# Optimization experiments

Hardware: AMD Instinct MI355X
Metric: run time of the kernel (lower is better)

Reference implementation:

```python
import jax, jax.numpy as jnp
import numpy as np

NUM_DST = 99
TUNNELS_PER_DST = 8
TOTAL_TUNNELS = NUM_DST * TUNNELS_PER_DST  # 792
NUM_LINKS = 16
BATCH = 65536
# static destination index of each tunnel (from group_sizes = [8]*99)
DEST_OF_TUNNEL = np.repeat(np.arange(NUM_DST), TUNNELS_PER_DST)  # [792]


def setup_inputs() -> dict:
    key = jax.random.key(0)
    k1, k2, k3, k4 = jax.random.split(key, 4)
    pred_ratios = jax.random.uniform(k1, (BATCH, TOTAL_TUNNELS), dtype=jnp.float32)
    demands = jax.random.uniform(k2, (BATCH, NUM_DST), dtype=jnp.float32)
    tunnel_to_link = jax.random.randint(k3, (TOTAL_TUNNELS,), 0, NUM_LINKS)
    link_capacities = jax.random.uniform(k4, (NUM_LINKS,), dtype=jnp.float32)
    return {
        "pred_ratios": pred_ratios,
        "demands": demands,
        "tunnel_to_link": tunnel_to_link,
        "link_capacities": link_capacities,
    }


def reference(pred_ratios, demands, tunnel_to_link, link_capacities):
    # per-tunnel traffic = demand of its destination * predicted split ratio
    tunnel_traffic = pred_ratios * demands[:, DEST_OF_TUNNEL]  # [B, T]
    # vectorized scatter-add over tunnels into links (replaces nested Python loops)
    link_traffic = jnp.zeros((pred_ratios.shape[0], NUM_LINKS), dtype=pred_ratios.dtype)
    link_traffic = link_traffic.at[:, tunnel_to_link].add(tunnel_traffic)  # [B, L]
    link_utilization = link_traffic / (link_capacities[None, :] + 1e-8)
    variance_loss = jnp.var(link_utilization, axis=1, ddof=1).mean()  # torch.var is unbiased
    max_util_loss = jnp.max(link_utilization, axis=1).mean()
    return variance_loss + 0.5 * max_util_loss
```

## Files before the change

kernel.cpp:

```cpp
#include <hip/hip_runtime.h>

#define T      792
#define ND     99
#define NL     16
#define KBLK   25
#define BATCH  65536
#define NTILES (BATCH / 16)

typedef __attribute__((ext_vector_type(8))) short  short8;
typedef __attribute__((ext_vector_type(4))) float  float4v;

__device__ inline unsigned short f2bf(float x) {
    union { float f; unsigned u; } c; c.f = x;
    unsigned r = (c.u + 0x7FFFu + ((c.u >> 16) & 1u)) >> 16;
    return (unsigned short)r;
}

__global__ __launch_bounds__(256) void llb_mfma(
    const float* __restrict__ pred,
    const float* __restrict__ dem,
    const int*   __restrict__ t2l,
    const float* __restrict__ cap,
    float* __restrict__ partial)
{
    __shared__ short8 Bfrag[KBLK][64];

    const int lane = threadIdx.x & 63;
    const int wid  = threadIdx.x >> 6;
    const int g    = lane >> 4;
    const int n    = lane & 15;

    for (int kb = wid; kb < KBLK; kb += 4) {
        const int k0 = kb * 32 + g * 8;
        union { unsigned short us[8]; short8 v; } b;
#pragma unroll
        for (int j = 0; j < 8; ++j) {
            const int k = k0 + j;
            const int link = (k < T) ? t2l[k] : -1;
            b.us[j] = (link == n) ? (unsigned short)0x3F80 : (unsigned short)0;
        }
        Bfrag[kb][lane] = b.v;
    }
    __syncthreads();

    const float invcap = 1.0f / (cap[n] + 1e-8f);

    const int tile = (int)blockIdx.x * 4 + wid;
    const int arow_i = tile * 16 + n;
    const float* __restrict__ arow = pred + (size_t)arow_i * T;
    const float* __restrict__ drow = dem  + (size_t)arow_i * ND;

    float4v acc = {0.f, 0.f, 0.f, 0.f};
#pragma unroll 5
    for (int kb = 0; kb < KBLK; ++kb) {
        const int k0 = kb * 32 + g * 8;
        const int kc = (k0 <= T - 8) ? k0 : (T - 8);
        int d0 = k0 >> 3;
        if (d0 > ND - 1) d0 = ND - 1;

        const float4v a0 = *(const float4v*)(arow + kc);
        const float4v a1 = *(const float4v*)(arow + kc + 4);
        const float   d  = drow[d0];

        union { unsigned short us[8]; short8 v; } af;
        af.us[0] = f2bf(a0.x * d); af.us[1] = f2bf(a0.y * d);
        af.us[2] = f2bf(a0.z * d); af.us[3] = f2bf(a0.w * d);
        af.us[4] = f2bf(a1.x * d); af.us[5] = f2bf(a1.y * d);
        af.us[6] = f2bf(a1.z * d); af.us[7] = f2bf(a1.w * d);

        acc = __builtin_amdgcn_mfma_f32_16x16x32_bf16(af.v, Bfrag[kb][lane], acc, 0, 0, 0);
    }

    float lsum = 0.f;
#pragma unroll
    for (int r = 0; r < 4; ++r) {
        const float u = acc[r] * invcap;
        float s = u, q = u * u, m = u;
#pragma unroll
        for (int off = 8; off >= 1; off >>= 1) {
            s += __shfl_xor(s, off, 16);
            q += __shfl_xor(q, off, 16);
            const float om = __shfl_xor(m, off, 16);
            m = m > om ? m : om;
        }
        if (n == 0) {
            const float var = (q - s * s * (1.0f / 16.0f)) * (1.0f / 15.0f);
            lsum += var + 0.5f * m;
        }
    }
    lsum += __shfl_xor(lsum, 16, 64);
    lsum += __shfl_xor(lsum, 32, 64);
    if (lane == 0) partial[tile] = lsum;
}

__global__ __launch_bounds__(256) void llb_reduce(
    const float* __restrict__ partial, float* __restrict__ out)
{
    float s = 0.f;
    for (int i = threadIdx.x; i < NTILES; i += 256) s += partial[i];
#pragma unroll
    for (int off = 32; off >= 1; off >>= 1) s += __shfl_xor(s, off, 64);
    __shared__ float red[4];
    if ((threadIdx.x & 63) == 0) red[threadIdx.x >> 6] = s;
    __syncthreads();
    if (threadIdx.x == 0)
        out[0] = (red[0] + red[1] + red[2] + red[3]) * (1.0f / (float)BATCH);
}

extern "C" void kernel_launch(void* const* d_in, const int* in_sizes, int n_in,
                              void* d_out, int out_size, void* d_ws, size_t ws_size,
                              hipStream_t stream) {
    const float* pred = (const float*)d_in[0];
    const float* dem  = (const float*)d_in[1];
    const int*   t2l  = (const int*)d_in[2];
    const float* cap  = (const float*)d_in[3];
    float* out     = (float*)d_out;
    float* partial = (float*)d_ws;

    llb_mfma<<<NTILES / 4, 256, 0, stream>>>(pred, dem, t2l, cap, partial);
    llb_reduce<<<1, 256, 0, stream>>>(partial, out);
}
```

Baseline: 324.1 us.

## Split K across wave pairs and pack tunnel-link map into nibbles

Each 16-row tile is now handled by two wavefronts, each covering half of the K blocks. The partial accumulators are combined through shared memory before the variance/max epilogue, and the grid size doubles. The one-hot B fragment is no longer held in shared memory; it is rebuilt in registers from a 4-bit-packed link map. This aims to expose more memory-level parallelism on a bandwidth-bound stream, at the cost of an extra block barrier, per-iteration compare ALU work, and half the waves idling in the epilogue.

Measured after the change: 319.4 us. No clear change (-1.4%).

```diff
diff --git a/kernel.cpp b/kernel.cpp
--- a/kernel.cpp
+++ b/kernel.cpp
@@ -12,8 +12,7 @@
 
 __device__ inline unsigned short f2bf(float x) {
     union { float f; unsigned u; } c; c.f = x;
-    unsigned r = (c.u + 0x7FFFu + ((c.u >> 16) & 1u)) >> 16;
-    return (unsigned short)r;
+    return (unsigned short)((c.u + 0x7FFFu + ((c.u >> 16) & 1u)) >> 16);
 }
 
 __global__ __launch_bounds__(256) void llb_mfma(
@@ -23,74 +22,84 @@
     const float* __restrict__ cap,
     float* __restrict__ partial)
 {
-    __shared__ short8 Bfrag[KBLK][64];
+    __shared__ unsigned packed[KBLK * 4];
+    __shared__ float4v  comb[2][64];
 
     const int lane = threadIdx.x & 63;
     const int wid  = threadIdx.x >> 6;
     const int g    = lane >> 4;
     const int n    = lane & 15;
 
-    for (int kb = wid; kb < KBLK; kb += 4) {
-        const int k0 = kb * 32 + g * 8;
-        union { unsigned short us[8]; short8 v; } b;
+    if (threadIdx.x < KBLK * 4) {
+        const int w = threadIdx.x;
+        unsigned u = 0;
 #pragma unroll
         for (int j = 0; j < 8; ++j) {
-            const int k = k0 + j;
-            const int link = (k < T) ? t2l[k] : -1;
-            b.us[j] = (link == n) ? (unsigned short)0x3F80 : (unsigned short)0;
+            const int k = w * 8 + j;
+            const unsigned link = (k < T) ? (unsigned)t2l[k] : 0u;
+            u |= link << (4 * j);
         }
-        Bfrag[kb][lane] = b.v;
+        packed[w] = u;
     }
     __syncthreads();
 
-    const float invcap = 1.0f / (cap[n] + 1e-8f);
-
-    const int tile = (int)blockIdx.x * 4 + wid;
+    const int tile   = (int)blockIdx.x * 2 + (wid >> 1);
+    const int kb0    = (wid & 1) ? 13 : 0;
+    const int kb1    = (wid & 1) ? KBLK : 13;
     const int arow_i = tile * 16 + n;
     const float* __restrict__ arow = pred + (size_t)arow_i * T;
     const float* __restrict__ drow = dem  + (size_t)arow_i * ND;
 
     float4v acc = {0.f, 0.f, 0.f, 0.f};
-#pragma unroll 5
-    for (int kb = 0; kb < KBLK; ++kb) {
-        const int k0 = kb * 32 + g * 8;
-        const int kc = (k0 <= T - 8) ? k0 : (T - 8);
-        int d0 = k0 >> 3;
-        if (d0 > ND - 1) d0 = ND - 1;
-
+#pragma unroll 4
+    for (int kb = kb0; kb < kb1; ++kb) {
+        const int idx = kb * 4 + g;
+        const int k0  = idx * 8;
+        const int kc  = (k0 <= T - 8) ? k0 : (T - 8);
         const float4v a0 = *(const float4v*)(arow + kc);
         const float4v a1 = *(const float4v*)(arow + kc + 4);
-        const float   d  = drow[d0];
+        const float   d  = (idx < ND) ? drow[idx] : 0.f;
+        const unsigned u = packed[idx];
 
-        union { unsigned short us[8]; short8 v; } af;
+        union { unsigned short us[8]; short8 v; } af, bf;
         af.us[0] = f2bf(a0.x * d); af.us[1] = f2bf(a0.y * d);
         af.us[2] = f2bf(a0.z * d); af.us[3] = f2bf(a0.w * d);
         af.us[4] = f2bf(a1.x * d); af.us[5] = f2bf(a1.y * d);
         af.us[6] = f2bf(a1.z * d); af.us[7] = f2bf(a1.w * d);
+#pragma unroll
+        for (int j = 0; j < 8; ++j)
+            bf.us[j] = (((u >> (4 * j)) & 15u) == (unsigned)n)
+                           ? (unsigned short)0x3F80 : (unsigned short)0;
 
-        acc = __builtin_amdgcn_mfma_f32_16x16x32_bf16(af.v, Bfrag[kb][lane], acc, 0, 0, 0);
+        acc = __builtin_amdgcn_mfma_f32_16x16x32_bf16(af.v, bf.v, acc, 0, 0, 0);
     }
 
-    float lsum = 0.f;
+    if (wid & 1) comb[wid >> 1][lane] = acc;
+    __syncthreads();
+    if (!(wid & 1)) {
+        const float4v o = comb[wid >> 1][lane];
+        const float invcap = 1.0f / (cap[n] + 1e-8f);
+        float lsum = 0.f;
 #pragma unroll
-    for (int r = 0; r < 4; ++r) {
-        const float u = acc[r] * invcap;
-        float s = u, q = u * u, m = u;
+        for (int r = 0; r < 4; ++r) {
+            const float uu = (acc[r] + o[r]) * invcap;
+            float s = uu, q = uu * uu, m = uu;
 #pragma unroll
-        for (int off = 8; off >= 1; off >>= 1) {
-            s += __shfl_xor(s, off, 16);
-            q += __shfl_xor(q, off, 16);
-            const float om = __shfl_xor(m, off, 16);
-            m = m > om ? m : om;
+            for (int off = 8; off >= 1; off >>= 1) {
+                s += __shfl_xor(s, off, 16);
+                q += __shfl_xor(q, off, 16);
+                const float om = __shfl_xor(m, off, 16);
+                m = m > om ? m : om;
+            }
+            if (n == 0) {
+                const float var = (q - s * s * (1.0f / 16.0f)) * (1.0f / 15.0f);
+                lsum += var + 0.5f * m;
+            }
         }
-        if (n == 0) {
-            const float var = (q - s * s * (1.0f / 16.0f)) * (1.0f / 15.0f);
-            lsum += var + 0.5f * m;
-        }
+        lsum += __shfl_xor(lsum, 16, 64);
+        lsum += __shfl_xor(lsum, 32, 64);
+        if (lane == 0) partial[tile] = lsum;
     }
-    lsum += __shfl_xor(lsum, 16, 64);
-    lsum += __shfl_xor(lsum, 32, 64);
-    if (lane == 0) partial[tile] = lsum;
 }
 
 __global__ __launch_bounds__(256) void llb_reduce(
@@ -117,6 +126,6 @@
     float* out     = (float*)d_out;
     float* partial = (float*)d_ws;
 
-    llb_mfma<<<NTILES / 4, 256, 0, stream>>>(pred, dem, t2l, cap, partial);
+    llb_mfma<<<NTILES / 2, 256, 0, stream>>>(pred, dem, t2l, cap, partial);
     llb_reduce<<<1, 256, 0, stream>>>(partial, out);
 }
```
